# Kernel optimization log

Measured on AMD Instinct MI355X. Metric: run time of the kernel, lower is better.

## Reference

```python
import jax, jax.numpy as jnp
import numpy as np

# MSDeformAttn-style fusion config (canonical deformable-DETR defaults)
D = 256      # d_model
NH = 8       # n_heads
NP = 4       # n_points per level
NL = 2       # n_levels (= num_feature_levels: modality v and modality i)
B, H, W = 4, 64, 64


def setup_inputs() -> dict:
    key = jax.random.key(0)
    ks = jax.random.split(key, 8)
    s = 0.02
    return {
        'input_v': jax.random.normal(ks[0], (B, D, H, W), jnp.float32),
        'input_i': jax.random.normal(ks[1], (B, D, H, W), jnp.float32),
        'W_value': jax.random.normal(ks[2], (D, D), jnp.float32) * s,
        'b_value': jnp.zeros((D,), jnp.float32),
        'W_off':   jax.random.normal(ks[3], (D, NH * NL * NP * 2), jnp.float32) * s,
        'b_off':   jax.random.normal(ks[4], (NH * NL * NP * 2,), jnp.float32) * s,
        'W_attn':  jax.random.normal(ks[5], (D, NH * NL * NP), jnp.float32) * s,
        'b_attn':  jnp.zeros((NH * NL * NP,), jnp.float32),
        'W_out':   jax.random.normal(ks[6], (D, D), jnp.float32) * s,
        'b_out':   jnp.zeros((D,), jnp.float32),
    }


def _bilinear_sample(value_l, locs, Hl, Wl):
    # value_l: (B, NH, HW, dh)  flattened per-level value
    # locs:    (B, Lq, NH, NP, 2) normalized sampling locations in [0,1]
    # returns  (B, NH, Lq, NP, dh); grid_sample semantics: zeros padding, align_corners=False
    b, nh, hw, dh = value_l.shape
    lq = locs.shape[1]
    x = locs[..., 0] * Wl - 0.5
    y = locs[..., 1] * Hl - 0.5
    x0 = jnp.floor(x)
    y0 = jnp.floor(y)
    dx = x - x0
    dy = y - y0
    x0i = x0.astype(jnp.int32)
    y0i = y0.astype(jnp.int32)
    out = jnp.zeros((b, nh, lq, NP, dh), value_l.dtype)
    corners = [
        (x0i,     y0i,     (1 - dx) * (1 - dy)),
        (x0i + 1, y0i,     dx * (1 - dy)),
        (x0i,     y0i + 1, (1 - dx) * dy),
        (x0i + 1, y0i + 1, dx * dy),
    ]
    for xi, yi, wgt in corners:
        valid = ((xi >= 0) & (xi < Wl) & (yi >= 0) & (yi < Hl)).astype(value_l.dtype)
        idx = jnp.clip(yi, 0, Hl - 1) * Wl + jnp.clip(xi, 0, Wl - 1)      # (B,Lq,NH,NP)
        idx_t = idx.transpose(0, 2, 1, 3).reshape(b, nh, lq * NP, 1)       # (B,NH,Lq*NP,1)
        g = jnp.take_along_axis(value_l, idx_t, axis=2)                    # (B,NH,Lq*NP,dh)
        g = g.reshape(b, nh, lq, NP, dh)
        w_t = (wgt * valid).transpose(0, 2, 1, 3)[..., None]               # (B,NH,Lq,NP,1)
        out = out + g * w_t
    return out


def reference(input_v, input_i, W_value, b_value, W_off, b_off, W_attn, b_attn, W_out, b_out):
    b, c, h, w = input_v.shape
    hw = h * w
    lq = NL * hw
    dh = c // NH

    # flatten both modalities into one token sequence (level 0 = v, level 1 = i)
    src_v = input_v.reshape(b, c, hw).transpose(0, 2, 1)
    src_i = input_i.reshape(b, c, hw).transpose(0, 2, 1)
    src = jnp.concatenate([src_v, src_i], axis=1)                          # (B, Lq, C)

    value = (src @ W_value + b_value).reshape(b, lq, NH, dh)
    value = value.transpose(0, 2, 1, 3)                                    # (B, NH, Lq, dh)
    value_levels = [value[:, :, :hw], value[:, :, hw:]]

    offsets = (src @ W_off + b_off).reshape(b, lq, NH, NL, NP, 2)
    attn = jax.nn.softmax((src @ W_attn + b_attn).reshape(b, lq, NH, NL * NP), axis=-1)
    attn = attn.reshape(b, lq, NH, NL, NP)

    # reference points: normalized pixel centers, same grid for both levels
    xs = (jnp.arange(w, dtype=jnp.float32) + 0.5) / w
    ys = (jnp.arange(h, dtype=jnp.float32) + 0.5) / h
    gy, gx = jnp.meshgrid(ys, xs, indexing='ij')
    ref = jnp.stack([gx.reshape(-1), gy.reshape(-1)], axis=-1)             # (HW, 2)
    ref = jnp.concatenate([ref, ref], axis=0)                              # (Lq, 2)

    norm = jnp.array([w, h], dtype=jnp.float32)
    locs = ref[None, :, None, None, None, :] + offsets / norm              # (B,Lq,NH,NL,NP,2)

    sampled = jnp.stack(
        [_bilinear_sample(value_levels[l], locs[:, :, :, l], h, w) for l in range(NL)],
        axis=3)                                                            # (B,NH,Lq,NL,NP,dh)

    fused = jnp.einsum('bqhlp,bhqlpd->bqhd', attn, sampled).reshape(b, lq, c)
    out = fused @ W_out + b_out                                            # (B, Lq, C)

    out_v = out[:, :hw]
    out_i = out[:, hw:]
    o = out_v + out_i                                                      # (B, HW, C)
    return o.transpose(0, 2, 1).reshape(b, c, h, w)
```

## Files before the change

kernel.cpp:

```cpp
#include <hip/hip_runtime.h>

#define HW 4096
#define LQ 8192
#define DD 256

typedef __bf16 bf16x8 __attribute__((ext_vector_type(8)));
typedef float  f32x4  __attribute__((ext_vector_type(4)));
typedef unsigned int u32;
typedef u32 u32x4 __attribute__((ext_vector_type(4)));

__device__ __forceinline__ float bflo(u32 u) { return __uint_as_float(u << 16); }
__device__ __forceinline__ float bfhi(u32 u) { return __uint_as_float(u & 0xffff0000u); }

#define GLOAD16(g, l) __builtin_amdgcn_global_load_lds(                     \
    (__attribute__((address_space(1))) void*)(g),                          \
    (__attribute__((address_space(3))) void*)(l), 16, 0, 0)

__global__ __launch_bounds__(256) void prep_all(const float* __restrict__ in_v,
                                                const float* __restrict__ in_i,
                                                const float* __restrict__ Wv,
                                                const float* __restrict__ Wo,
                                                const float* __restrict__ Wa,
                                                const float* __restrict__ Wout,
                                                char* __restrict__ srcS,
                                                char* __restrict__ WcatT,
                                                char* __restrict__ WoutT)
{
    __shared__ float tile[64][68];
    if (blockIdx.z < 8) {
        const int q0 = blockIdx.x * 64;
        const int k0 = blockIdx.y * 64;
        const int bz = blockIdx.z;
        const float* src = ((bz & 1) ? in_i : in_v) + (size_t)(bz >> 1) * (DD * HW);
        const int t  = threadIdx.x;
        const int ql = (t & 15) * 4;
        const int kl = t >> 4;
#pragma unroll
        for (int rr = 0; rr < 4; ++rr) {
            const float4 v = *(const float4*)(src + (size_t)(k0 + kl + rr * 16) * HW + q0 + ql);
            *(float4*)&tile[kl + rr * 16][ql] = v;
        }
        __syncthreads();
        const int qrow = t >> 2;
        const int kc   = (t & 3) * 16;
        const int row  = (bz >> 1) * LQ + (bz & 1) * HW + q0 + qrow;
        bf16x8 p0, p1;
#pragma unroll
        for (int j = 0; j < 8; ++j) {
            p0[j] = (__bf16)tile[kc + j][qrow];
            p1[j] = (__bf16)tile[kc + 8 + j][qrow];
        }
        char* drow = srcS + (size_t)row * 512;
        const int sw   = (row & 7) << 4;
        const int base = k0 * 2 + kc * 2;
        *(bf16x8*)(drow + ((base)      ^ sw)) = p0;
        *(bf16x8*)(drow + ((base + 16) ^ sw)) = p1;
    } else {
        const int flat = blockIdx.y * 64 + blockIdx.x;
        if (flat >= 120) return;
        const int gi = flat * 256 + threadIdx.x;
        if (gi < 448 * 32) {
            const int row = gi >> 5;
            const int g   = gi & 31;
            const int k   = g * 8;
            const float* col; int stride;
            if (row < 256)      { col = Wv + row;         stride = 256; }
            else if (row < 384) { col = Wo + (row - 256); stride = 128; }
            else                { col = Wa + (row - 384); stride = 64;  }
            bf16x8 p;
#pragma unroll
            for (int j = 0; j < 8; ++j) p[j] = (__bf16)col[(size_t)(k + j) * stride];
            char* d = WcatT + (size_t)row * 512;
            *(bf16x8*)(d + ((g * 16) ^ ((row & 7) << 4))) = p;
        } else {
            const int gj = gi - 448 * 32;
            if (gj >= 256 * 64) return;
            const int c = gj >> 6;
            const int g = gj & 63;
            const int k = (g * 8) & 255;
            bf16x8 p;
#pragma unroll
            for (int j = 0; j < 8; ++j) p[j] = (__bf16)Wout[(size_t)(k + j) * 256 + c];
            char* d = WoutT + (size_t)c * 1024;
            *(bf16x8*)(d + ((g * 16) ^ ((c & 7) << 4))) = p;
        }
    }
}

__global__ __launch_bounds__(256) void mfma_proj(const char* __restrict__ srcS,
                                                 const char* __restrict__ WcatT,
                                                 const float* __restrict__ b_value,
                                                 const float* __restrict__ b_off,
                                                 const float* __restrict__ b_attn,
                                                 __bf16* __restrict__ valueB,
                                                 __bf16* __restrict__ offB,
                                                 __bf16* __restrict__ attnB)
{
    __shared__ char smem[24576];
    char* As = smem;
    char* Bs = smem + 16384;

    const int M0 = blockIdx.x * 128;
    const int N0 = blockIdx.y * 64;
    const int t = threadIdx.x;
    const int w = t >> 6;
    const int l = t & 63;
    const int lm = l & 15, lk = l >> 4;
    const int wave_m = (w >> 1) * 64;
    const int wave_n = (w & 1) * 32;

    f32x4 acc[4][2] = {};

    const char* Ab = As + (wave_m + lm) * 128;
    const char* Bb = Bs + (wave_n + lm) * 128;
    const int go0 = (lk ^ (l & 7)) * 16;
    const int go1 = go0 ^ 64;

    for (int kt = 0; kt < 4; ++kt) {
        __syncthreads();
        const int kb = kt * 128;
#pragma unroll
        for (int c = 0; c < 4; ++c) {
            const char* g = srcS + (size_t)(M0 + w * 32 + c * 8 + (l >> 3)) * 512 + kb + (l & 7) * 16;
            GLOAD16(g, As + (w * 4 + c) * 1024);
        }
#pragma unroll
        for (int c = 0; c < 2; ++c) {
            const char* g = WcatT + (size_t)(N0 + w * 16 + c * 8 + (l >> 3)) * 512 + kb + (l & 7) * 16;
            GLOAD16(g, Bs + (w * 2 + c) * 1024);
        }
        __syncthreads();

        bf16x8 af[4], bb[2];
#pragma unroll
        for (int mi = 0; mi < 4; ++mi) af[mi] = *(const bf16x8*)(Ab + mi * 2048 + go0);
#pragma unroll
        for (int ni = 0; ni < 2; ++ni) bb[ni] = *(const bf16x8*)(Bb + ni * 2048 + go0);
#pragma unroll
        for (int mi = 0; mi < 4; ++mi)
#pragma unroll
            for (int ni = 0; ni < 2; ++ni)
                acc[mi][ni] = __builtin_amdgcn_mfma_f32_16x16x32_bf16(af[mi], bb[ni], acc[mi][ni], 0, 0, 0);
#pragma unroll
        for (int mi = 0; mi < 4; ++mi) af[mi] = *(const bf16x8*)(Ab + mi * 2048 + go1);
#pragma unroll
        for (int ni = 0; ni < 2; ++ni) bb[ni] = *(const bf16x8*)(Bb + ni * 2048 + go1);
#pragma unroll
        for (int mi = 0; mi < 4; ++mi)
#pragma unroll
            for (int ni = 0; ni < 2; ++ni)
                acc[mi][ni] = __builtin_amdgcn_mfma_f32_16x16x32_bf16(af[mi], bb[ni], acc[mi][ni], 0, 0, 0);
    }

    if (N0 < 256) {
#pragma unroll
        for (int ni = 0; ni < 2; ++ni) {
            const int cl = N0 + wave_n + ni * 16 + lm;
            const float bv = b_value[cl];
#pragma unroll
            for (int mi = 0; mi < 4; ++mi) {
                const int row = M0 + wave_m + mi * 16 + lk * 4;
#pragma unroll
                for (int r = 0; r < 4; ++r)
                    valueB[(size_t)(row + r) * 256 + cl] = (__bf16)(acc[mi][ni][r] + bv);
            }
        }
    } else if (N0 < 384) {
#pragma unroll
        for (int ni = 0; ni < 2; ++ni) {
            const int cl = (N0 - 256) + wave_n + ni * 16 + lm;
            const float bv = b_off[cl];
#pragma unroll
            for (int mi = 0; mi < 4; ++mi) {
                const int row = M0 + wave_m + mi * 16 + lk * 4;
#pragma unroll
                for (int r = 0; r < 4; ++r)
                    offB[(size_t)(row + r) * 128 + cl] = (__bf16)(acc[mi][ni][r] + bv);
            }
        }
    } else {
#pragma unroll
        for (int ni = 0; ni < 2; ++ni) {
            const int cl = wave_n + ni * 16 + lm;
            const float bv = b_attn[cl];
#pragma unroll
            for (int mi = 0; mi < 4; ++mi) {
                const int row = M0 + wave_m + mi * 16 + lk * 4;
#pragma unroll
                for (int r = 0; r < 4; ++r)
                    attnB[(size_t)(row + r) * 64 + cl] = (__bf16)(acc[mi][ni][r] + bv);
            }
        }
    }
}

__global__ __launch_bounds__(256) void sample_kernel(const char* __restrict__ valueB,
                                                     const char* __restrict__ offB,
                                                     const char* __restrict__ attnB,
                                                     char* __restrict__ fusedS)
{
    const int bid  = blockIdx.x;
    const int w    = threadIdx.x >> 6;
    const int lane = threadIdx.x & 63;
    const int q2   = lane >> 5;
    const int sub  = lane & 31;
    const int head = sub >> 2;
    const int d8   = (sub & 3) << 3;

    const int px   = bid & 15;
    const int py   = (bid >> 4) & 31;
    const int half = (bid >> 9) & 1;
    const int b    = bid >> 10;
    const int x    = px * 4 + (w & 1) * 2 + q2;
    const int y    = py * 2 + (w >> 1);
    const int row  = b * LQ + half * HW + y * 64 + x;
    const float fx0 = (float)x;
    const float fy0 = (float)y;

    const u32x4 lgp = *(const u32x4*)(attnB + (size_t)row * 128 + head * 16);
    float e[8];
#pragma unroll
    for (int j = 0; j < 4; ++j) { e[2 * j] = bflo(lgp[j]); e[2 * j + 1] = bfhi(lgp[j]); }
    float mx = e[0];
#pragma unroll
    for (int j = 1; j < 8; ++j) mx = fmaxf(mx, e[j]);
    float s = 0.f;
#pragma unroll
    for (int j = 0; j < 8; ++j) { e[j] = __expf(e[j] - mx); s += e[j]; }
    const float inv = 1.0f / s;

    const char* ofp = offB + (size_t)row * 256 + head * 32;
    const u32x4 o0 = *(const u32x4*)ofp;
    const u32x4 o1 = *(const u32x4*)(ofp + 16);
    float o[16];
#pragma unroll
    for (int j = 0; j < 4; ++j) {
        o[2 * j]     = bflo(o0[j]); o[2 * j + 1] = bfhi(o0[j]);
        o[8 + 2 * j] = bflo(o1[j]); o[9 + 2 * j] = bfhi(o1[j]);
    }

    float acc[8] = {};
#pragma unroll
    for (int ll = 0; ll < 2; ++ll) {
        const char* vb = valueB + (((size_t)(b * LQ + ll * HW)) << 9) + head * 64 + d8 * 2;
#pragma unroll
        for (int p = 0; p < 4; ++p) {
            const float ox = o[ll * 8 + p * 2];
            const float oy = o[ll * 8 + p * 2 + 1];
            const float aw = e[ll * 4 + p] * inv;
            const float xx = fx0 + ox;
            const float yy = fy0 + oy;
            const float xf = floorf(xx), yf = floorf(yy);
            const int   xi = (int)xf,   yi = (int)yf;
            const float dx = xx - xf,   dy = yy - yf;
            float w00 = (1.f - dx) * (1.f - dy);
            float w10 = dx * (1.f - dy);
            float w01 = (1.f - dx) * dy;
            float w11 = dx * dy;
            const bool vx0 = (unsigned)xi       < 64u;
            const bool vx1 = (unsigned)(xi + 1) < 64u;
            const bool vy0 = (unsigned)yi       < 64u;
            const bool vy1 = (unsigned)(yi + 1) < 64u;
            const float u00 = (vx0 && vy0) ? aw * w00 : 0.f;
            const float u10 = (vx1 && vy0) ? aw * w10 : 0.f;
            const float u01 = (vx0 && vy1) ? aw * w01 : 0.f;
            const float u11 = (vx1 && vy1) ? aw * w11 : 0.f;
            const int xc0 = min(max(xi, 0), 63);
            const int xc1 = min(max(xi + 1, 0), 63);
            const int yc0 = min(max(yi, 0), 63) << 6;
            const int yc1 = min(max(yi + 1, 0), 63) << 6;
            const u32x4 g00 = *(const u32x4*)(vb + ((size_t)(yc0 + xc0) << 9));
            const u32x4 g10 = *(const u32x4*)(vb + ((size_t)(yc0 + xc1) << 9));
            const u32x4 g01 = *(const u32x4*)(vb + ((size_t)(yc1 + xc0) << 9));
            const u32x4 g11 = *(const u32x4*)(vb + ((size_t)(yc1 + xc1) << 9));
#pragma unroll
            for (int j = 0; j < 4; ++j) {
                acc[2 * j]     += u00 * bflo(g00[j]) + u10 * bflo(g10[j]) + u01 * bflo(g01[j]) + u11 * bflo(g11[j]);
                acc[2 * j + 1] += u00 * bfhi(g00[j]) + u10 * bfhi(g10[j]) + u01 * bfhi(g01[j]) + u11 * bfhi(g11[j]);
            }
        }
    }
    bf16x8 ov;
#pragma unroll
    for (int j = 0; j < 8; ++j) ov[j] = (__bf16)acc[j];
    const int bo = (head * 64 + d8 * 2) ^ ((row & 7) << 4);
    *(bf16x8*)(fusedS + (size_t)row * 512 + bo) = ov;
}

__global__ __launch_bounds__(256) void mfma_out(const char* __restrict__ fusedS,
                                                const char* __restrict__ WoutT,
                                                const float* __restrict__ b_out,
                                                float* __restrict__ out)
{
    __shared__ char smem[24576];
    char* As = smem;
    char* Bs = smem + 16384;
    float* Tr = (float*)smem;

    const int M0 = blockIdx.x * 128;
    const int N0 = blockIdx.y * 64;
    const int bi = M0 >> 12;
    const int q0 = M0 & 4095;
    const int t = threadIdx.x;
    const int w = t >> 6;
    const int l = t & 63;
    const int lm = l & 15, lk = l >> 4;
    const int wave_m = (w >> 1) * 64;
    const int wave_n = (w & 1) * 32;

    f32x4 acc[4][2] = {};

    const char* Ab = As + (wave_m + lm) * 128;
    const char* Bb = Bs + (wave_n + lm) * 128;
    const int go0 = (lk ^ (l & 7)) * 16;
    const int go1 = go0 ^ 64;

    for (int kt = 0; kt < 8; ++kt) {
        __syncthreads();
        const int half = kt >> 2;
        const int kb   = (kt & 3) * 128;
#pragma unroll
        for (int c = 0; c < 4; ++c) {
            const char* g = fusedS + (size_t)(bi * LQ + half * HW + q0 + w * 32 + c * 8 + (l >> 3)) * 512
                          + kb + (l & 7) * 16;
            GLOAD16(g, As + (w * 4 + c) * 1024);
        }
#pragma unroll
        for (int c = 0; c < 2; ++c) {
            const char* g = WoutT + (size_t)(N0 + w * 16 + c * 8 + (l >> 3)) * 1024 + kt * 128 + (l & 7) * 16;
            GLOAD16(g, Bs + (w * 2 + c) * 1024);
        }
        __syncthreads();

        bf16x8 af[4], bb[2];
#pragma unroll
        for (int mi = 0; mi < 4; ++mi) af[mi] = *(const bf16x8*)(Ab + mi * 2048 + go0);
#pragma unroll
        for (int ni = 0; ni < 2; ++ni) bb[ni] = *(const bf16x8*)(Bb + ni * 2048 + go0);
#pragma unroll
        for (int mi = 0; mi < 4; ++mi)
#pragma unroll
            for (int ni = 0; ni < 2; ++ni)
                acc[mi][ni] = __builtin_amdgcn_mfma_f32_16x16x32_bf16(af[mi], bb[ni], acc[mi][ni], 0, 0, 0);
#pragma unroll
        for (int mi = 0; mi < 4; ++mi) af[mi] = *(const bf16x8*)(Ab + mi * 2048 + go1);
#pragma unroll
        for (int ni = 0; ni < 2; ++ni) bb[ni] = *(const bf16x8*)(Bb + ni * 2048 + go1);
#pragma unroll
        for (int mi = 0; mi < 4; ++mi)
#pragma unroll
            for (int ni = 0; ni < 2; ++ni)
                acc[mi][ni] = __builtin_amdgcn_mfma_f32_16x16x32_bf16(af[mi], bb[ni], acc[mi][ni], 0, 0, 0);
    }

    float bias2[2];
#pragma unroll
    for (int ni = 0; ni < 2; ++ni) bias2[ni] = 2.0f * b_out[N0 + wave_n + ni * 16 + lm];

#pragma unroll
    for (int h = 0; h < 2; ++h) {
        __syncthreads();
        if ((w >> 1) == h) {
#pragma unroll
            for (int mi = 0; mi < 4; ++mi)
#pragma unroll
                for (int ni = 0; ni < 2; ++ni)
#pragma unroll
                    for (int r = 0; r < 4; ++r)
                        Tr[(wave_n + ni * 16 + lm) * 68 + mi * 16 + lk * 4 + r] = acc[mi][ni][r] + bias2[ni];
        }
        __syncthreads();
        const int c  = t >> 2;
        const int qo = (t & 3) * 16;
        float* dst = out + ((size_t)(bi * DD + N0 + c)) * HW + q0 + h * 64 + qo;
        const float* sp = Tr + c * 68 + qo;
#pragma unroll
        for (int j = 0; j < 4; ++j)
            *(f32x4*)(dst + j * 4) = *(const f32x4*)(sp + j * 4);
    }
}

extern "C" void kernel_launch(void* const* d_in, const int* in_sizes, int n_in,
                              void* d_out, int out_size, void* d_ws, size_t ws_size,
                              hipStream_t stream) {
    const float* in_v    = (const float*)d_in[0];
    const float* in_i    = (const float*)d_in[1];
    const float* W_value = (const float*)d_in[2];
    const float* b_value = (const float*)d_in[3];
    const float* W_off   = (const float*)d_in[4];
    const float* b_off   = (const float*)d_in[5];
    const float* W_attn  = (const float*)d_in[6];
    const float* b_attn  = (const float*)d_in[7];
    const float* W_out   = (const float*)d_in[8];
    const float* b_out   = (const float*)d_in[9];
    float* out = (float*)d_out;

    char* ws = (char*)d_ws;
    __bf16* valueB = (__bf16*)(ws);
    __bf16* offB   = (__bf16*)(ws + 16777216);
    __bf16* attnB  = (__bf16*)(ws + 25165824);
    char*   srcS   = ws + 29360128;
    char*   fusedS = ws + 46137344;
    char*   WcatT  = ws + 62914560;
    char*   WoutT  = ws + 63143936;

    prep_all<<<dim3(64, 4, 9), 256, 0, stream>>>(in_v, in_i, W_value, W_off, W_attn, W_out,
                                                 srcS, WcatT, WoutT);
    mfma_proj<<<dim3(256, 7), 256, 0, stream>>>(srcS, WcatT, b_value, b_off, b_attn,
                                                valueB, offB, attnB);
    sample_kernel<<<dim3(4096), 256, 0, stream>>>((const char*)valueB, (const char*)offB,
                                                  (const char*)attnB, fusedS);
    mfma_out<<<dim3(128, 4), 256, 0, stream>>>(fusedS, WoutT, b_out, out);
}
```

Baseline: 78.71 us.

## Split bilinear weight/index computation across lanes via LDS and remap block order

```diff
diff --git a/kernel.cpp b/kernel.cpp
--- a/kernel.cpp
+++ b/kernel.cpp
@@ -8,6 +8,7 @@
 typedef float  f32x4  __attribute__((ext_vector_type(4)));
 typedef unsigned int u32;
 typedef u32 u32x4 __attribute__((ext_vector_type(4)));
+typedef u32 u32x2 __attribute__((ext_vector_type(2)));
 
 __device__ __forceinline__ float bflo(u32 u) { return __uint_as_float(u << 16); }
 __device__ __forceinline__ float bfhi(u32 u) { return __uint_as_float(u & 0xffff0000u); }
@@ -199,13 +200,15 @@
                                                      const char* __restrict__ attnB,
                                                      char* __restrict__ fusedS)
 {
-    const int bid  = blockIdx.x;
+    __shared__ u32 wlds[4][128][8];
+    const int bid0 = blockIdx.x;
+    const int bid  = ((bid0 & 7) << 9) | (bid0 >> 3);
     const int w    = threadIdx.x >> 6;
     const int lane = threadIdx.x & 63;
     const int q2   = lane >> 5;
     const int sub  = lane & 31;
     const int head = sub >> 2;
-    const int d8   = (sub & 3) << 3;
+    const int dl   = sub & 3;
 
     const int px   = bid & 15;
     const int py   = (bid >> 4) & 31;
@@ -218,68 +221,74 @@
     const float fy0 = (float)y;
 
     const u32x4 lgp = *(const u32x4*)(attnB + (size_t)row * 128 + head * 16);
-    float e[8];
-#pragma unroll
-    for (int j = 0; j < 4; ++j) { e[2 * j] = bflo(lgp[j]); e[2 * j + 1] = bfhi(lgp[j]); }
-    float mx = e[0];
-#pragma unroll
-    for (int j = 1; j < 8; ++j) mx = fmaxf(mx, e[j]);
-    float s = 0.f;
-#pragma unroll
-    for (int j = 0; j < 8; ++j) { e[j] = __expf(e[j] - mx); s += e[j]; }
-    const float inv = 1.0f / s;
-
-    const char* ofp = offB + (size_t)row * 256 + head * 32;
-    const u32x4 o0 = *(const u32x4*)ofp;
-    const u32x4 o1 = *(const u32x4*)(ofp + 16);
-    float o[16];
-#pragma unroll
-    for (int j = 0; j < 4; ++j) {
-        o[2 * j]     = bflo(o0[j]); o[2 * j + 1] = bfhi(o0[j]);
-        o[8 + 2 * j] = bflo(o1[j]); o[9 + 2 * j] = bfhi(o1[j]);
-    }
-
+    float e8[8];
+#pragma unroll
+    for (int j = 0; j < 4; ++j) { e8[2 * j] = bflo(lgp[j]); e8[2 * j + 1] = bfhi(lgp[j]); }
+    float mx = e8[0];
+#pragma unroll
+    for (int j = 1; j < 8; ++j) mx = fmaxf(mx, e8[j]);
+    const int pt0 = dl * 2;
+    const float ex0 = __expf(e8[pt0] - mx);
+    const float ex1 = __expf(e8[pt0 + 1] - mx);
+    float sp = ex0 + ex1;
+    sp += __shfl_xor(sp, 1);
+    sp += __shfl_xor(sp, 2);
+    const float inv = 1.0f / sp;
+
+    const u32x2 opk = *(const u32x2*)(offB + (size_t)row * 256 + head * 32 + dl * 8);
+    u32* slotp = &wlds[w][q2 * 64 + head * 8 + pt0][0];
+#pragma unroll
+    for (int i = 0; i < 2; ++i) {
+        const float ox = bflo(opk[i]);
+        const float oy = bfhi(opk[i]);
+        const float aw = (i ? ex1 : ex0) * inv;
+        const float xx = fx0 + ox;
+        const float yy = fy0 + oy;
+        const float xf = floorf(xx), yf = floorf(yy);
+        const int   xi = (int)xf,   yi = (int)yf;
+        const float dx = xx - xf,   dy = yy - yf;
+        const bool vx0 = (unsigned)xi       < 64u;
+        const bool vx1 = (unsigned)(xi + 1) < 64u;
+        const bool vy0 = (unsigned)yi       < 64u;
+        const bool vy1 = (unsigned)(yi + 1) < 64u;
+        f32x4 W;
+        W[0] = (vx0 && vy0) ? aw * (1.f - dx) * (1.f - dy) : 0.f;
+        W[1] = (vx1 && vy0) ? aw * dx * (1.f - dy)         : 0.f;
+        W[2] = (vx0 && vy1) ? aw * (1.f - dx) * dy         : 0.f;
+        W[3] = (vx1 && vy1) ? aw * dx * dy                 : 0.f;
+        const int xc0 = min(max(xi, 0), 63);
+        const int xc1 = min(max(xi + 1, 0), 63);
+        const int yc0 = min(max(yi, 0), 63) << 6;
+        const int yc1 = min(max(yi + 1, 0), 63) << 6;
+        const int lvl = ((pt0 + i) >> 2) * HW;
+        u32x4 S;
+        S[0] = lvl + yc0 + xc0; S[1] = lvl + yc0 + xc1;
+        S[2] = lvl + yc1 + xc0; S[3] = lvl + yc1 + xc1;
+        *(f32x4*)(slotp + i * 8)     = W;
+        *(u32x4*)(slotp + i * 8 + 4) = S;
+    }
+
+    const int d8 = dl << 3;
+    const char* vb = valueB + (((size_t)(b * LQ)) << 9) + head * 64 + d8 * 2;
+    const u32* slotb = &wlds[w][q2 * 64 + head * 8][0];
     float acc[8] = {};
-#pragma unroll
-    for (int ll = 0; ll < 2; ++ll) {
-        const char* vb = valueB + (((size_t)(b * LQ + ll * HW)) << 9) + head * 64 + d8 * 2;
-#pragma unroll
-        for (int p = 0; p < 4; ++p) {
-            const float ox = o[ll * 8 + p * 2];
-            const float oy = o[ll * 8 + p * 2 + 1];
-            const float aw = e[ll * 4 + p] * inv;
-            const float xx = fx0 + ox;
-            const float yy = fy0 + oy;
-            const float xf = floorf(xx), yf = floorf(yy);
-            const int   xi = (int)xf,   yi = (int)yf;
-            const float dx = xx - xf,   dy = yy - yf;
-            float w00 = (1.f - dx) * (1.f - dy);
-            float w10 = dx * (1.f - dy);
-            float w01 = (1.f - dx) * dy;
-            float w11 = dx * dy;
-            const bool vx0 = (unsigned)xi       < 64u;
-            const bool vx1 = (unsigned)(xi + 1) < 64u;
-            const bool vy0 = (unsigned)yi       < 64u;
-            const bool vy1 = (unsigned)(yi + 1) < 64u;
-            const float u00 = (vx0 && vy0) ? aw * w00 : 0.f;
-            const float u10 = (vx1 && vy0) ? aw * w10 : 0.f;
-            const float u01 = (vx0 && vy1) ? aw * w01 : 0.f;
-            const float u11 = (vx1 && vy1) ? aw * w11 : 0.f;
-            const int xc0 = min(max(xi, 0), 63);
-            const int xc1 = min(max(xi + 1, 0), 63);
-            const int yc0 = min(max(yi, 0), 63) << 6;
-            const int yc1 = min(max(yi + 1, 0), 63) << 6;
-            const u32x4 g00 = *(const u32x4*)(vb + ((size_t)(yc0 + xc0) << 9));
-            const u32x4 g10 = *(const u32x4*)(vb + ((size_t)(yc0 + xc1) << 9));
-            const u32x4 g01 = *(const u32x4*)(vb + ((size_t)(yc1 + xc0) << 9));
-            const u32x4 g11 = *(const u32x4*)(vb + ((size_t)(yc1 + xc1) << 9));
-#pragma unroll
-            for (int j = 0; j < 4; ++j) {
-                acc[2 * j]     += u00 * bflo(g00[j]) + u10 * bflo(g10[j]) + u01 * bflo(g01[j]) + u11 * bflo(g11[j]);
-                acc[2 * j + 1] += u00 * bfhi(g00[j]) + u10 * bfhi(g10[j]) + u01 * bfhi(g01[j]) + u11 * bfhi(g11[j]);
-            }
-        }
-    }
+    __builtin_amdgcn_s_setprio(1);
+#pragma unroll
+    for (int pt = 0; pt < 8; ++pt) {
+        const f32x4 W = *(const f32x4*)(slotb + pt * 8);
+        const u32x4 S = *(const u32x4*)(slotb + pt * 8 + 4);
+        const u32x4 g00 = *(const u32x4*)(vb + ((size_t)S[0] << 9));
+        const u32x4 g10 = *(const u32x4*)(vb + ((size_t)S[1] << 9));
+        const u32x4 g01 = *(const u32x4*)(vb + ((size_t)S[2] << 9));
+        const u32x4 g11 = *(const u32x4*)(vb + ((size_t)S[3] << 9));
+#pragma unroll
+        for (int j = 0; j < 4; ++j) {
+            acc[2 * j]     += W[0] * bflo(g00[j]) + W[1] * bflo(g10[j]) + W[2] * bflo(g01[j]) + W[3] * bflo(g11[j]);
+            acc[2 * j + 1] += W[0] * bfhi(g00[j]) + W[1] * bfhi(g10[j]) + W[2] * bfhi(g01[j]) + W[3] * bfhi(g11[j]);
+        }
+    }
+    __builtin_amdgcn_s_setprio(0);
+
     bf16x8 ov;
 #pragma unroll
     for (int j = 0; j < 8; ++j) ov[j] = (__bf16)acc[j];
```

Result: faster. 76.80 us (-2.4%).
